# Kernel optimization log

Hardware: AMD Instinct MI355X
Metric: run time of the kernel (lower is better)

The kernel has to match this reference:

```python
import jax, jax.numpy as jnp
import numpy as np

# ContextualAttention config (matches init_kwargs)
KS, STRIDE, DIL, FUSE_K, SCALE = 3, 1, 1, 3, 10.0
B, C, H, W = 2, 128, 64, 64
L = H * W  # number of background patches (SAME padding, stride 1)


def _same_pad(x, k, s):
    # TF-style SAME padding, identical to the repo's same_padding helper
    _, _, h, w = x.shape
    oh, ow = -(-h // s), -(-w // s)
    ph = max(0, (oh - 1) * s + k - h)
    pw = max(0, (ow - 1) * s + k - w)
    return jnp.pad(x, ((0, 0), (0, 0), (ph // 2, ph - ph // 2), (pw // 2, pw - pw // 2)))


def _patches(x, k, s):
    # extract_image_patches: SAME pad + unfold -> [N, L, C*k*k], (c, kh, kw) ordering
    xp = _same_pad(x, k, s)
    n, c, hp, wp = xp.shape
    oh, ow = (hp - k) // s + 1, (wp - k) // s + 1
    cols = jnp.stack(
        [xp[:, :, i:i + (oh - 1) * s + 1:s, j:j + (ow - 1) * s + 1:s]
         for i in range(k) for j in range(k)], axis=2)  # [N, C, k*k, oh, ow]
    return cols.reshape(n, c * k * k, oh * ow).transpose(0, 2, 1)


def _fuse(scores):
    # diagonal fuse-smoothing: conv the [L_b, L_f] score matrix with eye(k), twice
    # (second pass on the transposed spatial layout), exactly as in the torch code
    bn = scores.shape[0]
    eye = jnp.eye(FUSE_K, dtype=scores.dtype)[None, None]  # [1,1,k,k]
    conv = lambda v: jax.lax.conv_general_dilated(
        v, eye, (1, 1), [(1, 1), (1, 1)],
        dimension_numbers=('NCHW', 'OIHW', 'NCHW'))
    y = conv(scores.reshape(bn, 1, L, L))
    y = y.reshape(bn, H, W, H, W).transpose(0, 2, 1, 4, 3).reshape(bn, 1, L, L)
    y = conv(y)
    y = y.reshape(bn, W, H, W, H).transpose(0, 2, 1, 4, 3)  # back to [b,H,W,H,W]
    return y.reshape(bn, L, H, W)


def setup_inputs() -> dict:
    key = jax.random.key(0)
    kf, kb, km = jax.random.split(key, 3)
    f = jax.random.normal(kf, (B, C, H, W), jnp.float32)
    b = jax.random.normal(kb, (B, C, H, W), jnp.float32)
    mask = (jax.random.uniform(km, (1, 1, H, W)) < 0.05).astype(jnp.float32)
    return {"f": f, "b": b, "mask": mask}


def reference(f, b, mask):
    kernel = 2 * DIL  # raw patch size for aggregation (=2)
    # raw background patches used by the transposed-conv aggregation
    raw_w = _patches(b, kernel, DIL * STRIDE).reshape(B, L, C, kernel, kernel)
    # DIL == 1 => F.interpolate(scale=1.0, nearest) is identity on f/b/mask
    w = _patches(b, KS, STRIDE)      # [B, L, C*9] matching patches
    fp = _patches(f, KS, 1)          # [B, Lf, C*9] foreground patches (SAME pad)
    m = _patches(mask, KS, STRIDE)[0]                    # [L, 9]
    mm = (jnp.mean(m, axis=1) == 0.0).astype(f.dtype)    # [L] 1 = patch usable

    # per-patch L2 normalization (clamped at 1e-4), conv-as-similarity == patch GEMM
    wn = w / jnp.maximum(jnp.sqrt(jnp.sum(w * w, axis=2, keepdims=True)), 1e-4)
    scores = jnp.einsum('bkd,bqd->bkq', wn, fp).reshape(B, L, H, W)
    scores = _fuse(scores)

    mmb = mm[None, :, None, None]
    attn = jax.nn.softmax(scores * mmb * SCALE, axis=1) * mmb  # softmax over L

    # conv_transpose2d(attn, raw_w, stride=1, padding=1) == VALID corr with flipped,
    # IO-swapped 2x2 kernel (k-1-p = 0 padding); per-sample weights -> vmap
    def agg(a, rw):  # a: [L,H,W], rw: [L,C,2,2]
        rhs = jnp.flip(rw, axis=(2, 3)).transpose(1, 0, 2, 3)  # [C, L, 2, 2] OIHW
        return jax.lax.conv_general_dilated(
            a[None], rhs, (1, 1), [(0, 0), (0, 0)],
            dimension_numbers=('NCHW', 'OIHW', 'NCHW'))[0]

    y = jax.vmap(agg)(attn, raw_w) / 4.0       # [B, C, H-1, W-1]
    y = jnp.pad(y, ((0, 0), (0, 0), (0, 1), (0, 1)))  # output_padding = DIL % 2 = 1
    return y
```

## Files before the change

kernel.cpp:

```cpp
#include <hip/hip_runtime.h>

#define L 4096
#define HH 64
#define CC 128
#define BB 2

typedef _Float16 f16;
typedef _Float16 f16x8 __attribute__((ext_vector_type(8)));
typedef float f32x4 __attribute__((ext_vector_type(4)));

__device__ __forceinline__ void gl_lds16(const f16* g, f16* l) {
  __builtin_amdgcn_global_load_lds(
      (const __attribute__((address_space(1))) void*)g,
      (__attribute__((address_space(3))) void*)l, 16, 0, 0);
}

__device__ __forceinline__ int sigma_(int j) { return ((j & 63) << 6) | (j >> 6); }

__device__ float fuse9(const f16* __restrict__ Sb, int k, int j) {
  float acc = 0.f;
  int cK = sigma_(k), cQ = sigma_(j);
#pragma unroll
  for (int u = -1; u <= 1; ++u) {
    int a = cK + u, bq = cQ + u;
    if ((unsigned)a < L && (unsigned)bq < L) {
      int r = sigma_(a), c = sigma_(bq);
#pragma unroll
      for (int t = -1; t <= 1; ++t) {
        int rr = r + t, cc = c + t;
        if ((unsigned)rr < L && (unsigned)cc < L) acc += (float)Sb[(size_t)rr * L + cc];
      }
    }
  }
  return acc;
}

__global__ __launch_bounds__(256) void k_repack(
    const float* __restrict__ b, const float* __restrict__ f,
    f16* __restrict__ bT, f16* __restrict__ fT, f16* __restrict__ zp) {
  __shared__ float tile[128][65];
  int u0 = blockIdx.x * 64;
  int z = blockIdx.y;
  int batch = z >> 1;
  const float* src = ((z & 1) ? f : b) + (size_t)batch * CC * L;
  f16* dst = ((z & 1) ? fT : bT) + (size_t)batch * L * CC;
  int tid = threadIdx.x;
  if (blockIdx.x == 0 && z == 0 && tid < 32) zp[tid] = (f16)0.f;
#pragma unroll
  for (int i = 0; i < 32; ++i) {
    int idx = i * 256 + tid;
    int c = idx >> 6, ux = idx & 63;
    tile[c][ux] = src[(size_t)c * L + u0 + ux];
  }
  __syncthreads();
#pragma unroll
  for (int j = 0; j < 4; ++j) {
    int t2 = j * 256 + tid;
    int u = t2 >> 4, ch = t2 & 15;
    f16x8 v;
#pragma unroll
    for (int e = 0; e < 8; ++e) v[e] = (f16)tile[ch * 8 + e][u];
    *(f16x8*)(dst + (size_t)(u0 + u) * CC + ch * 8) = v;
  }
}

__global__ __launch_bounds__(256) void k_ssq(const float* __restrict__ b, float* __restrict__ ssq) {
  int u = blockIdx.x * 256 + threadIdx.x;
  int batch = blockIdx.y;
  const float* bp = b + (size_t)batch * CC * L + u;
  float s = 0.f;
#pragma unroll 4
  for (int c = 0; c < CC; ++c) { float v = bp[(size_t)c * L]; s += v * v; }
  ssq[batch * L + u] = s;
}

__global__ void k_norm(const float* __restrict__ ssq, float* __restrict__ inv_n) {
  int gi = blockIdx.x * 256 + threadIdx.x;
  if (gi >= BB * L) return;
  int batch = gi >> 12, k = gi & (L - 1);
  int ky = k >> 6, kx = k & 63;
  float s = 0.f;
#pragma unroll
  for (int dy = -1; dy <= 1; ++dy)
#pragma unroll
    for (int dx = -1; dx <= 1; ++dx) {
      if ((unsigned)(ky + dy) < 64 && (unsigned)(kx + dx) < 64)
        s += ssq[batch * L + k + dy * 64 + dx];
    }
  inv_n[gi] = 1.f / fmaxf(sqrtf(s), 1e-4f);
}

__global__ __launch_bounds__(256) void k_prep_bm(const float* __restrict__ b, f16* __restrict__ bm) {
  int idx = blockIdx.x * 256 + threadIdx.x;
  int e8 = idx * 8;
  int k0 = e8 & (L - 1);
  int c = (e8 >> 12) & (CC - 1);
  int bt = e8 >> 19;
  int batch = bt & 1;
  int tap = bt >> 1;
  int di = 1 - (tap >> 1), dj = 1 - (tap & 1);
  int ky = k0 >> 6, kx0 = k0 & 63;
  const float* src = b + ((size_t)batch * CC + c) * L + k0 + di * 64 + dj;
  bool rowok = (ky + di) < 64;
  f16x8 v;
#pragma unroll
  for (int e = 0; e < 8; ++e) {
    float x = (rowok && (kx0 + e + dj) < 64) ? src[e] : 0.f;
    v[e] = (f16)x;
  }
  *(f16x8*)(bm + (size_t)e8) = v;
}

__global__ void k_prep_mm(const float* __restrict__ mask, float* __restrict__ mmv) {
  int k = blockIdx.x * 256 + threadIdx.x;
  if (k >= L) return;
  int ky = k >> 6, kx = k & 63;
  float s = 0.f;
  for (int i = 0; i < 3; ++i)
    for (int j = 0; j < 3; ++j) {
      int yy = ky + i - 1, xx = kx + j - 1;
      if (yy >= 0 && yy < 64 && xx >= 0 && xx < 64) s += mask[yy * 64 + xx];
    }
  mmv[k] = (s == 0.f) ? 1.f : 0.f;
}

__global__ void k_zcnt(const float* __restrict__ mmv, float* __restrict__ zcnt) {
  int i = blockIdx.x * 256 + threadIdx.x;
  if (i >= 512) return;
  float s = 0.f;
#pragma unroll
  for (int r = 0; r < 8; ++r) s += (mmv[i * 8 + r] == 0.f) ? 1.f : 0.f;
  zcnt[i] = s;
}

__global__ __launch_bounds__(256) void k_gemm_scores(
    const f16* __restrict__ bT, const f16* __restrict__ fT,
    const float* __restrict__ inv_n, const f16* __restrict__ zp,
    f16* __restrict__ S) {
  __shared__ f16 As[2][128 * 64];
  __shared__ f16 Bs[2][128 * 64];
  int qt = blockIdx.x, kt = blockIdx.y, batch = blockIdx.z;
  int tid = threadIdx.x, wid = tid >> 6, lane = tid & 63;
  int wr = wid >> 1, wc = wid & 1;
  const f16* A0 = bT + (size_t)batch * L * CC;
  const f16* B0 = fT + (size_t)batch * L * CC;
  f32x4 acc[4][4] = {};
  int rA = wr * 64 + (lane & 15);
  int rB = wc * 64 + (lane & 15);

  const f16* baseA_[4]; const f16* baseB_[4];
  int offL_[4];
  unsigned mA_[4], mB_[4];
#pragma unroll
  for (int i = 0; i < 4; ++i) {
    int chunk = (i * 4 + wid) * 64 + lane;
    int row = chunk >> 3;
    int lg = (lane & 7) ^ (row & 7);
    int k = kt * 128 + row;
    int q = qt * 128 + row;
    baseA_[i] = A0 + (size_t)k * CC + lg * 8;
    baseB_[i] = B0 + (size_t)q * CC + lg * 8;
    offL_[i] = chunk * 8;
    int ky = k >> 6, kx = k & 63, qy = q >> 6, qx = q & 63;
    unsigned ma = 0, mb = 0;
#pragma unroll
    for (int rr = 0; rr < 9; ++rr) {
      int dy = rr / 3 - 1, dx = rr - (rr / 3) * 3 - 1;
      if ((unsigned)(ky + dy) < 64u && (unsigned)(kx + dx) < 64u) ma |= 1u << rr;
      if ((unsigned)(qy + dy) < 64u && (unsigned)(qx + dx) < 64u) mb |= 1u << rr;
    }
    mA_[i] = ma; mB_[i] = mb;
  }

#define STAGE_T(tt, bsel)                                                     \
  do {                                                                        \
    int rr_ = (tt) >> 1, half_ = (tt) & 1;                                    \
    int dy_ = rr_ / 3 - 1, dx_ = rr_ - (rr_ / 3) * 3 - 1;                     \
    int doff_ = (dy_ * 64 + dx_) * CC + half_ * 64;                           \
    _Pragma("unroll")                                                         \
    for (int i = 0; i < 4; ++i) {                                             \
      gl_lds16(((mA_[i] >> rr_) & 1u) ? (baseA_[i] + doff_) : zp,             \
               &As[bsel][0] + offL_[i]);                                      \
      gl_lds16(((mB_[i] >> rr_) & 1u) ? (baseB_[i] + doff_) : zp,             \
               &Bs[bsel][0] + offL_[i]);                                      \
    }                                                                         \
  } while (0)

  STAGE_T(0, 0);
  int cur = 0;
#pragma unroll 1
  for (int t = 0; t < 18; ++t) {
    __syncthreads();
    if (t < 17) STAGE_T(t + 1, cur ^ 1);
    const f16* Ab = &As[cur][0];
    const f16* Bb = &Bs[cur][0];
#pragma unroll
    for (int h2 = 0; h2 < 2; ++h2) {
      int cb = h2 * 4 + (lane >> 4);
      f16x8 af[4], bf[4];
#pragma unroll
      for (int m = 0; m < 4; ++m) {
        int row = rA + m * 16;
        af[m] = *(const f16x8*)(Ab + row * 64 + ((cb ^ (row & 7)) * 8));
      }
#pragma unroll
      for (int n = 0; n < 4; ++n) {
        int row = rB + n * 16;
        bf[n] = *(const f16x8*)(Bb + row * 64 + ((cb ^ (row & 7)) * 8));
      }
#pragma unroll
      for (int m = 0; m < 4; ++m)
#pragma unroll
        for (int n = 0; n < 4; ++n)
          acc[m][n] = __builtin_amdgcn_mfma_f32_16x16x32_f16(af[m], bf[n], acc[m][n], 0, 0, 0);
    }
    cur ^= 1;
  }
#undef STAGE_T

  f16* Srow = S + (size_t)batch * L * L;
  int kbase = kt * 128 + wr * 64 + (lane >> 4) * 4;
  int qbase = qt * 128 + wc * 64 + (lane & 15);
#pragma unroll
  for (int m = 0; m < 4; ++m) {
    f32x4 invv = *(const f32x4*)(inv_n + (size_t)batch * L + kbase + m * 16);
#pragma unroll
    for (int r = 0; r < 4; ++r) {
      f16* dst = Srow + (size_t)(kbase + m * 16 + r) * L + qbase;
#pragma unroll
      for (int n = 0; n < 4; ++n) dst[n * 16] = (f16)(acc[m][n][r] * invv[r]);
    }
  }
}

__global__ __launch_bounds__(256) void k_fuse_stats(
    const f16* __restrict__ S, const float* __restrict__ mmv,
    f16* __restrict__ P, float* __restrict__ pmP, float* __restrict__ pl) {
  int tid = threadIdx.x;
  if (tid >= 247) return;
  int jc = blockIdx.x, kc = blockIdx.y, batch = blockIdx.z;
  int g = jc * 247 + tid;
  int q0 = 72 + g * 8;
  const f16* Sb = S + (size_t)batch * L * L;
  f16* Pb = P + (size_t)batch * L * L;
  float lg[8][8];
  float m8[8];
#pragma unroll
  for (int e = 0; e < 8; ++e) m8[e] = -3.0e38f;
  unsigned vmask = 0;
  int k0 = kc * 8;
#pragma unroll
  for (int kk = 0; kk < 8; ++kk) {
    int k = k0 + kk;
    if (mmv[k] == 0.f) continue;
    vmask |= 1u << kk;
    float acc[8] = {0.f, 0.f, 0.f, 0.f, 0.f, 0.f, 0.f, 0.f};
    int cK = sigma_(k);
#pragma unroll
    for (int u = -1; u <= 1; ++u) {
      int a = cK + u;
      if ((unsigned)a >= L) continue;
      int r = sigma_(a);
      const f16* cb = Sb + (size_t)r * L + (q0 + 64 * u);
      {
        f16x8 v = *(const f16x8*)cb;
#pragma unroll
        for (int e = 0; e < 8; ++e) acc[e] += (float)v[e];
      }
      if (r >= 1) {
        const f16* rm = cb - L;
        f16x8 v = *(const f16x8*)rm;
        acc[0] += (float)rm[-1];
#pragma unroll
        for (int e = 1; e < 8; ++e) acc[e] += (float)v[e - 1];
      }
      if (r <= L - 2) {
        const f16* rp = cb + L;
        f16x8 v = *(const f16x8*)rp;
#pragma unroll
        for (int e = 0; e < 7; ++e) acc[e] += (float)v[e + 1];
        acc[7] += (float)rp[8];
      }
    }
#pragma unroll
    for (int e = 0; e < 8; ++e) {
      float x = acc[e] * 10.f;
      lg[kk][e] = x;
      m8[e] = fmaxf(m8[e], x);
    }
  }
  float l8[8] = {0.f, 0.f, 0.f, 0.f, 0.f, 0.f, 0.f, 0.f};
#pragma unroll
  for (int kk = 0; kk < 8; ++kk) {
    if (!((vmask >> kk) & 1u)) continue;
    f16 v[8];
#pragma unroll
    for (int e = 0; e < 8; ++e) {
      float p = __expf(lg[kk][e] - m8[e]);
      l8[e] += p;
      v[e] = (f16)p;
    }
    *(f16x8*)(Pb + (size_t)(k0 + kk) * L + q0) = *(f16x8*)v;
  }
  float* pmp = pmP + (size_t)kc * (BB * L) + (size_t)batch * L + q0;
  float* plp = pl + (size_t)kc * (BB * L) + (size_t)batch * L + q0;
  *(f32x4*)pmp = *(f32x4*)&m8[0]; *(f32x4*)(pmp + 4) = *(f32x4*)&m8[4];
  *(f32x4*)plp = *(f32x4*)&l8[0]; *(f32x4*)(plp + 4) = *(f32x4*)&l8[4];
}

__global__ __launch_bounds__(256) void k_fuse_stats_edge(
    const f16* __restrict__ S, const float* __restrict__ mmv,
    f16* __restrict__ P, float* __restrict__ pmP, float* __restrict__ pl) {
  int tid = threadIdx.x;
  if (tid >= 144) return;
  int q = (tid < 72) ? tid : (4024 + tid - 72);
  int kc = blockIdx.x, batch = blockIdx.y;
  const f16* Sb = S + (size_t)batch * L * L;
  f16* Pb = P + (size_t)batch * L * L;
  float lgs[8];
  float m = -3.0e38f;
  unsigned vmask = 0;
  int k0 = kc * 8;
#pragma unroll
  for (int kk = 0; kk < 8; ++kk) {
    int k = k0 + kk;
    if (mmv[k] == 0.f) continue;
    vmask |= 1u << kk;
    float x = 10.f * fuse9(Sb, k, q);
    lgs[kk] = x;
    m = fmaxf(m, x);
  }
  float l = 0.f;
#pragma unroll
  for (int kk = 0; kk < 8; ++kk) {
    if (!((vmask >> kk) & 1u)) continue;
    float p = __expf(lgs[kk] - m);
    l += p;
    Pb[(size_t)(k0 + kk) * L + q] = (f16)p;
  }
  pmP[(size_t)kc * (BB * L) + (size_t)batch * L + q] = m;
  pl[(size_t)kc * (BB * L) + (size_t)batch * L + q] = l;
}

__global__ __launch_bounds__(256) void k_softmax_reduce(
    const float* __restrict__ pmP, const float* __restrict__ pl,
    const float* __restrict__ zcnt,
    float* __restrict__ Mq, float* __restrict__ invLq) {
  __shared__ float sm[4][64], sl[4][64];
  int tid = threadIdx.x;
  int ql = tid & 63, part = tid >> 6;
  int qi = blockIdx.x * 64 + ql;
  float m = -3.0e38f, l = 0.f;
  int i0 = part * 128;
  float cntp = 0.f;
#pragma unroll 4
  for (int i = i0; i < i0 + 128; ++i) {
    float pmv = pmP[(size_t)i * (BB * L) + qi];
    float plv = pl[(size_t)i * (BB * L) + qi];
    float nm = fmaxf(m, pmv);
    l = l * __expf(m - nm) + plv * __expf(pmv - nm);
    m = nm;
    cntp += zcnt[i & 511];
  }
  if (cntp > 0.f) {
    float nm = fmaxf(m, 0.f);
    l = l * __expf(m - nm) + cntp * __expf(-nm);
    m = nm;
  }
  sm[part][ql] = m; sl[part][ql] = l;
  __syncthreads();
  if (part == 0) {
    float M = sm[0][ql];
#pragma unroll
    for (int p = 1; p < 4; ++p) M = fmaxf(M, sm[p][ql]);
    float Ls = 0.f;
#pragma unroll
    for (int p = 0; p < 4; ++p) Ls += sl[p][ql] * __expf(sm[p][ql] - M);
    Mq[qi] = M;
    invLq[qi] = 1.f / Ls;
  }
}

__global__ __launch_bounds__(512) void k_agg(
    const f16* __restrict__ P, const float* __restrict__ pmP,
    const float* __restrict__ mmv,
    const float* __restrict__ Mq, const float* __restrict__ invLq,
    const f16* __restrict__ bm, float* __restrict__ part) {
  __shared__ f16 Asm[512 * 32];
  __shared__ f16 Bt[136 * 40];
  int pt = blockIdx.x, ks = blockIdx.y, batch = blockIdx.z;
  int p0 = pt * 64;
  int tid = threadIdx.x, wid = tid >> 6, lane = tid & 63;
  int wr = wid >> 1, wc = wid & 1;
  const f16* Pb = P + (size_t)batch * L * L;

  const f16* gA_[4]; f16* lA_[4];
#pragma unroll
  for (int i = 0; i < 4; ++i) {
    int R = wid * 64 + i * 16 + (lane >> 2);
    int tap = R >> 7, c = R & 127;
    int chl = (lane & 3) ^ ((R >> 1) & 3);
    gA_[i] = bm + (((size_t)(tap * 2 + batch) * CC + c) * L) + chl * 8;
    lA_[i] = Asm + R * 32 + (lane & 3) * 8;
  }

  bool act1 = (tid < 32);
  int kg_[2]; bool qok_[2]; float M_[2], iL_[2];
  const f16* tb_[2]; f16* bw_[2];
  size_t bq_[2];
#pragma unroll
  for (int s = 0; s < 2; ++s) {
    int tau = tid + s * 512;
    int ppv = tau % 136, kgv = tau / 136;
    if (tau >= 544) { ppv = 0; kgv = 0; }
    kg_[s] = kgv;
    int q = p0 + ppv;
    bool qok = q < L;
    int qc = qok ? q : (L - 1);
    qok_[s] = qok;
    M_[s] = Mq[(size_t)batch * L + qc];
    iL_[s] = invLq[(size_t)batch * L + qc];
    tb_[s] = Pb + (size_t)(kgv * 8) * L + qc;
    bq_[s] = (size_t)batch * L + qc;
    bw_[s] = Bt + ppv * 40 + ((kgv ^ ((ppv >> 3) & 3)) * 8);
  }

  f16x8 vv_[2];
  int kend = ks * 1024 + 1024;

#define LOADB(K0)                                                             \
  do {                                                                        \
    _Pragma("unroll")                                                         \
    for (int s = 0; s < 2; ++s) {                                             \
      if (s == 1 && !act1) break;                                             \
      const f16* tp = tb_[s] + (size_t)(K0) * L;                              \
      int ck = ((K0) >> 3) + kg_[s];                                          \
      float pmv = pmP[(size_t)ck * (BB * L) + bq_[s]];                        \
      float corr = qok_[s] ? __expf(pmv - M_[s]) * iL_[s] : 0.f;              \
      f32x4 ma = *(const f32x4*)(mmv + (K0) + kg_[s] * 8);                    \
      f32x4 mb = *(const f32x4*)(mmv + (K0) + kg_[s] * 8 + 4);                \
      f16 pv[8];                                                              \
      _Pragma("unroll")                                                       \
      for (int j = 0; j < 8; ++j) pv[j] = tp[(size_t)j * L];                  \
      f16 v[8];                                                               \
      _Pragma("unroll")                                                       \
      for (int j = 0; j < 8; ++j) {                                           \
        float mmj = (j < 4) ? ma[j] : mb[j - 4];                              \
        v[j] = (mmj != 0.f) ? (f16)((float)pv[j] * corr) : (f16)0.f;          \
      }                                                                       \
      vv_[s] = *(f16x8*)v;                                                    \
    }                                                                         \
  } while (0)

  LOADB(ks * 1024);
  f32x4 acc[2][2] = {};
#pragma unroll 1
  for (int k0 = ks * 1024; k0 < kend; k0 += 32) {
    __syncthreads();
    *(f16x8*)bw_[0] = vv_[0];
    if (act1) *(f16x8*)bw_[1] = vv_[1];
#pragma unroll
    for (int i = 0; i < 4; ++i) gl_lds16(gA_[i] + k0, lA_[i]);
    __syncthreads();
#pragma unroll
    for (int tap = 0; tap < 4; ++tap) {
      int dlt = (tap >> 1) * 64 + (tap & 1);
      f16x8 af[2], bf[2];
#pragma unroll
      for (int m = 0; m < 2; ++m) {
        int R = tap * 128 + wr * 32 + m * 16 + (lane & 15);
        int ph = (lane >> 4) ^ ((R >> 1) & 3);
        af[m] = *(const f16x8*)(Asm + R * 32 + ph * 8);
      }
#pragma unroll
      for (int n = 0; n < 2; ++n) {
        int pp = wc * 32 + n * 16 + (lane & 15) + dlt;
        int ph = (lane >> 4) ^ ((pp >> 3) & 3);
        bf[n] = *(const f16x8*)(Bt + pp * 40 + ph * 8);
      }
#pragma unroll
      for (int m = 0; m < 2; ++m)
#pragma unroll
        for (int n = 0; n < 2; ++n)
          acc[m][n] = __builtin_amdgcn_mfma_f32_16x16x32_f16(af[m], bf[n], acc[m][n], 0, 0, 0);
    }
    if (k0 + 32 < kend) LOADB(k0 + 32);
  }
#undef LOADB

  int cb = wr * 32 + (lane >> 4) * 4;
  int pb = p0 + wc * 32 + (lane & 15);
#pragma unroll
  for (int m = 0; m < 2; ++m)
#pragma unroll
    for (int n = 0; n < 2; ++n)
#pragma unroll
      for (int r = 0; r < 4; ++r) {
        int c = cb + m * 16 + r;
        int p = pb + n * 16;
        part[(((size_t)ks * 2 + batch) * CC + c) * L + p] = acc[m][n][r];
      }
}

__global__ __launch_bounds__(256) void k_agg_reduce(const float* __restrict__ part, float* __restrict__ out) {
  int idx = (blockIdx.x * 256 + threadIdx.x) * 4;
  f32x4 s = {0.f, 0.f, 0.f, 0.f};
#pragma unroll
  for (int ks = 0; ks < 4; ++ks) {
    f32x4 v = *(const f32x4*)(part + (size_t)ks * (2 * CC * L) + idx);
#pragma unroll
    for (int e = 0; e < 4; ++e) s[e] += v[e];
  }
  int p = idx & (L - 1);
  int u = p >> 6, vv = p & 63;
  f32x4 o;
#pragma unroll
  for (int e = 0; e < 4; ++e) o[e] = (u < 63 && (vv + e) < 63) ? s[e] * 0.25f : 0.f;
  *(f32x4*)(out + idx) = o;
}

extern "C" void kernel_launch(void* const* d_in, const int* in_sizes, int n_in,
                              void* d_out, int out_size, void* d_ws, size_t ws_size,
                              hipStream_t stream) {
  const float* f = (const float*)d_in[0];
  const float* b = (const float*)d_in[1];
  const float* mask = (const float*)d_in[2];
  float* out = (float*)d_out;
  char* ws = (char*)d_ws;

  f16* P     = (f16*)(ws + 0);
  f16* S     = (f16*)(ws + 67108864);
  f16* bm    = (f16*)(ws + 134217728);
  float* part= (float*)(ws + 142606336);
  float* pmP = (float*)(ws + 159383552);
  float* pl  = (float*)(ws + 176160768);
  float* mmv = (float*)(ws + 192937984);
  float* Mq  = (float*)(ws + 192954368);
  float* iLq = (float*)(ws + 192987136);
  f16* bT    = (f16*)(ws + 193019904);
  f16* fT    = (f16*)(ws + 195117056);
  float* ssq = (float*)(ws + 197214208);
  float* invn= (float*)(ws + 197246976);
  f16* zp    = (f16*)(ws + 197279744);
  float* zcnt= (float*)(ws + 197279872);

  k_repack<<<dim3(64, 4), dim3(256), 0, stream>>>(b, f, bT, fT, zp);
  k_ssq<<<dim3(16, 2), dim3(256), 0, stream>>>(b, ssq);
  k_norm<<<dim3(32), dim3(256), 0, stream>>>(ssq, invn);
  k_prep_bm<<<dim3(2048), dim3(256), 0, stream>>>(b, bm);
  k_prep_mm<<<dim3(16), dim3(256), 0, stream>>>(mask, mmv);
  k_zcnt<<<dim3(2), dim3(256), 0, stream>>>(mmv, zcnt);
  k_gemm_scores<<<dim3(32, 32, 2), dim3(256), 0, stream>>>(bT, fT, invn, zp, S);
  k_fuse_stats<<<dim3(2, 512, 2), dim3(256), 0, stream>>>(S, mmv, P, pmP, pl);
  k_fuse_stats_edge<<<dim3(512, 2), dim3(256), 0, stream>>>(S, mmv, P, pmP, pl);
  k_softmax_reduce<<<dim3(128), dim3(256), 0, stream>>>(pmP, pl, zcnt, Mq, iLq);
  k_agg<<<dim3(64, 4, 2), dim3(512), 0, stream>>>(P, pmP, mmv, Mq, iLq, bm, part);
  k_agg_reduce<<<dim3(1024), dim3(256), 0, stream>>>(part, out);
}
```

Before: 310.4 us.

## Store softmax numerators transposed so aggregation loads contiguous 8-wide vectors

The fuse/stats kernels now write the exponentiated score matrix transposed ([q][k]), with masked entries written as explicit zeros. Each thread loops over 8 key chunks so it can emit 16-byte vector stores along k. The aggregation kernel's B-tile loader becomes a single f16x8 load per thread instead of eight strided scalar loads, and the mask reads are dropped. The cost is that the fuse kernel now writes strided rows (one row per q) and has 8x fewer blocks, each doing more serial work.

```diff
diff --git a/kernel.cpp b/kernel.cpp
--- a/kernel.cpp
+++ b/kernel.cpp
@@ -235,111 +235,133 @@
 
 __global__ __launch_bounds__(256) void k_fuse_stats(
     const f16* __restrict__ S, const float* __restrict__ mmv,
-    f16* __restrict__ P, float* __restrict__ pmP, float* __restrict__ pl) {
+    f16* __restrict__ PT, float* __restrict__ pmP, float* __restrict__ pl) {
   int tid = threadIdx.x;
   if (tid >= 247) return;
-  int jc = blockIdx.x, kc = blockIdx.y, batch = blockIdx.z;
+  int jc = blockIdx.x, kb = blockIdx.y, batch = blockIdx.z;
   int g = jc * 247 + tid;
   int q0 = 72 + g * 8;
   const f16* Sb = S + (size_t)batch * L * L;
-  f16* Pb = P + (size_t)batch * L * L;
-  float lg[8][8];
-  float m8[8];
-#pragma unroll
-  for (int e = 0; e < 8; ++e) m8[e] = -3.0e38f;
-  unsigned vmask = 0;
-  int k0 = kc * 8;
-#pragma unroll
-  for (int kk = 0; kk < 8; ++kk) {
-    int k = k0 + kk;
-    if (mmv[k] == 0.f) continue;
-    vmask |= 1u << kk;
-    float acc[8] = {0.f, 0.f, 0.f, 0.f, 0.f, 0.f, 0.f, 0.f};
-    int cK = sigma_(k);
-#pragma unroll
-    for (int u = -1; u <= 1; ++u) {
-      int a = cK + u;
-      if ((unsigned)a >= L) continue;
-      int r = sigma_(a);
-      const f16* cb = Sb + (size_t)r * L + (q0 + 64 * u);
-      {
-        f16x8 v = *(const f16x8*)cb;
-#pragma unroll
-        for (int e = 0; e < 8; ++e) acc[e] += (float)v[e];
-      }
-      if (r >= 1) {
-        const f16* rm = cb - L;
-        f16x8 v = *(const f16x8*)rm;
-        acc[0] += (float)rm[-1];
-#pragma unroll
-        for (int e = 1; e < 8; ++e) acc[e] += (float)v[e - 1];
-      }
-      if (r <= L - 2) {
-        const f16* rp = cb + L;
-        f16x8 v = *(const f16x8*)rp;
-#pragma unroll
-        for (int e = 0; e < 7; ++e) acc[e] += (float)v[e + 1];
-        acc[7] += (float)rp[8];
+  f16* Pb = PT + (size_t)batch * L * L;
+#pragma unroll 1
+  for (int sc = 0; sc < 8; ++sc) {
+    int k0 = kb * 64 + sc * 8;
+    float lg[8][8];
+    float m8[8];
+#pragma unroll
+    for (int e = 0; e < 8; ++e) m8[e] = -3.0e38f;
+    unsigned vmask = 0;
+#pragma unroll
+    for (int kk = 0; kk < 8; ++kk) {
+      int k = k0 + kk;
+      if (mmv[k] == 0.f) continue;
+      vmask |= 1u << kk;
+      float acc[8] = {0.f, 0.f, 0.f, 0.f, 0.f, 0.f, 0.f, 0.f};
+      int cK = sigma_(k);
+#pragma unroll
+      for (int u = -1; u <= 1; ++u) {
+        int a = cK + u;
+        if ((unsigned)a >= L) continue;
+        int r = sigma_(a);
+        const f16* cb = Sb + (size_t)r * L + (q0 + 64 * u);
+        {
+          f16x8 v = *(const f16x8*)cb;
+#pragma unroll
+          for (int e = 0; e < 8; ++e) acc[e] += (float)v[e];
+        }
+        if (r >= 1) {
+          const f16* rm = cb - L;
+          f16x8 v = *(const f16x8*)rm;
+          acc[0] += (float)rm[-1];
+#pragma unroll
+          for (int e = 1; e < 8; ++e) acc[e] += (float)v[e - 1];
+        }
+        if (r <= L - 2) {
+          const f16* rp = cb + L;
+          f16x8 v = *(const f16x8*)rp;
+#pragma unroll
+          for (int e = 0; e < 7; ++e) acc[e] += (float)v[e + 1];
+          acc[7] += (float)rp[8];
+        }
+      }
+#pragma unroll
+      for (int e = 0; e < 8; ++e) {
+        float x = acc[e] * 10.f;
+        lg[kk][e] = x;
+        m8[e] = fmaxf(m8[e], x);
+      }
+    }
+    float l8[8] = {0.f, 0.f, 0.f, 0.f, 0.f, 0.f, 0.f, 0.f};
+#pragma unroll
+    for (int kk = 0; kk < 8; ++kk) {
+      if ((vmask >> kk) & 1u) {
+#pragma unroll
+        for (int e = 0; e < 8; ++e) {
+          float p = __expf(lg[kk][e] - m8[e]);
+          l8[e] += p;
+          lg[kk][e] = p;
+        }
+      } else {
+#pragma unroll
+        for (int e = 0; e < 8; ++e) lg[kk][e] = 0.f;
       }
     }
 #pragma unroll
     for (int e = 0; e < 8; ++e) {
-      float x = acc[e] * 10.f;
-      lg[kk][e] = x;
-      m8[e] = fmaxf(m8[e], x);
-    }
-  }
-  float l8[8] = {0.f, 0.f, 0.f, 0.f, 0.f, 0.f, 0.f, 0.f};
-#pragma unroll
-  for (int kk = 0; kk < 8; ++kk) {
-    if (!((vmask >> kk) & 1u)) continue;
-    f16 v[8];
-#pragma unroll
-    for (int e = 0; e < 8; ++e) {
-      float p = __expf(lg[kk][e] - m8[e]);
-      l8[e] += p;
-      v[e] = (f16)p;
-    }
-    *(f16x8*)(Pb + (size_t)(k0 + kk) * L + q0) = *(f16x8*)v;
-  }
-  float* pmp = pmP + (size_t)kc * (BB * L) + (size_t)batch * L + q0;
-  float* plp = pl + (size_t)kc * (BB * L) + (size_t)batch * L + q0;
-  *(f32x4*)pmp = *(f32x4*)&m8[0]; *(f32x4*)(pmp + 4) = *(f32x4*)&m8[4];
-  *(f32x4*)plp = *(f32x4*)&l8[0]; *(f32x4*)(plp + 4) = *(f32x4*)&l8[4];
+      f16 v[8];
+#pragma unroll
+      for (int kk = 0; kk < 8; ++kk) v[kk] = (f16)lg[kk][e];
+      *(f16x8*)(Pb + (size_t)(q0 + e) * L + k0) = *(f16x8*)v;
+    }
+    int ck = kb * 8 + sc;
+    float* pmp = pmP + (size_t)ck * (BB * L) + (size_t)batch * L + q0;
+    float* plp = pl + (size_t)ck * (BB * L) + (size_t)batch * L + q0;
+    *(f32x4*)pmp = *(f32x4*)&m8[0]; *(f32x4*)(pmp + 4) = *(f32x4*)&m8[4];
+    *(f32x4*)plp = *(f32x4*)&l8[0]; *(f32x4*)(plp + 4) = *(f32x4*)&l8[4];
+  }
 }
 
 __global__ __launch_bounds__(256) void k_fuse_stats_edge(
     const f16* __restrict__ S, const float* __restrict__ mmv,
-    f16* __restrict__ P, float* __restrict__ pmP, float* __restrict__ pl) {
+    f16* __restrict__ PT, float* __restrict__ pmP, float* __restrict__ pl) {
   int tid = threadIdx.x;
   if (tid >= 144) return;
   int q = (tid < 72) ? tid : (4024 + tid - 72);
-  int kc = blockIdx.x, batch = blockIdx.y;
+  int kb = blockIdx.x, batch = blockIdx.y;
   const f16* Sb = S + (size_t)batch * L * L;
-  f16* Pb = P + (size_t)batch * L * L;
-  float lgs[8];
-  float m = -3.0e38f;
-  unsigned vmask = 0;
-  int k0 = kc * 8;
-#pragma unroll
-  for (int kk = 0; kk < 8; ++kk) {
-    int k = k0 + kk;
-    if (mmv[k] == 0.f) continue;
-    vmask |= 1u << kk;
-    float x = 10.f * fuse9(Sb, k, q);
-    lgs[kk] = x;
-    m = fmaxf(m, x);
-  }
-  float l = 0.f;
-#pragma unroll
-  for (int kk = 0; kk < 8; ++kk) {
-    if (!((vmask >> kk) & 1u)) continue;
-    float p = __expf(lgs[kk] - m);
-    l += p;
-    Pb[(size_t)(k0 + kk) * L + q] = (f16)p;
-  }
-  pmP[(size_t)kc * (BB * L) + (size_t)batch * L + q] = m;
-  pl[(size_t)kc * (BB * L) + (size_t)batch * L + q] = l;
+  f16* Pb = PT + (size_t)batch * L * L;
+#pragma unroll 1
+  for (int sc = 0; sc < 8; ++sc) {
+    int k0 = kb * 64 + sc * 8;
+    float lgs[8];
+    float m = -3.0e38f;
+    unsigned vmask = 0;
+#pragma unroll
+    for (int kk = 0; kk < 8; ++kk) {
+      int k = k0 + kk;
+      if (mmv[k] == 0.f) continue;
+      vmask |= 1u << kk;
+      float x = 10.f * fuse9(Sb, k, q);
+      lgs[kk] = x;
+      m = fmaxf(m, x);
+    }
+    float l = 0.f;
+    f16 v[8];
+#pragma unroll
+    for (int kk = 0; kk < 8; ++kk) {
+      if ((vmask >> kk) & 1u) {
+        float p = __expf(lgs[kk] - m);
+        l += p;
+        v[kk] = (f16)p;
+      } else {
+        v[kk] = (f16)0.f;
+      }
+    }
+    *(f16x8*)(Pb + (size_t)q * L + k0) = *(f16x8*)v;
+    int ck = kb * 8 + sc;
+    pmP[(size_t)ck * (BB * L) + (size_t)batch * L + q] = m;
+    pl[(size_t)ck * (BB * L) + (size_t)batch * L + q] = l;
+  }
 }
 
 __global__ __launch_bounds__(256) void k_softmax_reduce(
@@ -382,8 +404,7 @@
 }
 
 __global__ __launch_bounds__(512) void k_agg(
-    const f16* __restrict__ P, const float* __restrict__ pmP,
-    const float* __restrict__ mmv,
+    const f16* __restrict__ PT, const float* __restrict__ pmP,
     const float* __restrict__ Mq, const float* __restrict__ invLq,
     const f16* __restrict__ bm, float* __restrict__ part) {
   __shared__ f16 Asm[512 * 32];
@@ -392,7 +413,7 @@
   int p0 = pt * 64;
   int tid = threadIdx.x, wid = tid >> 6, lane = tid & 63;
   int wr = wid >> 1, wc = wid & 1;
-  const f16* Pb = P + (size_t)batch * L * L;
+  const f16* Pb = PT + (size_t)batch * L * L;
 
   const f16* gA_[4]; f16* lA_[4];
 #pragma unroll
@@ -406,12 +427,12 @@
 
   bool act1 = (tid < 32);
   int kg_[2]; bool qok_[2]; float M_[2], iL_[2];
-  const f16* tb_[2]; f16* bw_[2];
+  const f16* ptb_[2]; f16* bw_[2];
   size_t bq_[2];
 #pragma unroll
   for (int s = 0; s < 2; ++s) {
     int tau = tid + s * 512;
-    int ppv = tau % 136, kgv = tau / 136;
+    int kgv = tau & 3, ppv = tau >> 2;
     if (tau >= 544) { ppv = 0; kgv = 0; }
     kg_[s] = kgv;
     int q = p0 + ppv;
@@ -420,7 +441,7 @@
     qok_[s] = qok;
     M_[s] = Mq[(size_t)batch * L + qc];
     iL_[s] = invLq[(size_t)batch * L + qc];
-    tb_[s] = Pb + (size_t)(kgv * 8) * L + qc;
+    ptb_[s] = Pb + (size_t)qc * L + kgv * 8;
     bq_[s] = (size_t)batch * L + qc;
     bw_[s] = Bt + ppv * 40 + ((kgv ^ ((ppv >> 3) & 3)) * 8);
   }
@@ -433,21 +454,13 @@
     _Pragma("unroll")                                                         \
     for (int s = 0; s < 2; ++s) {                                             \
       if (s == 1 && !act1) break;                                             \
-      const f16* tp = tb_[s] + (size_t)(K0) * L;                              \
+      f16x8 pv = *(const f16x8*)(ptb_[s] + (K0));                             \
       int ck = ((K0) >> 3) + kg_[s];                                          \
       float pmv = pmP[(size_t)ck * (BB * L) + bq_[s]];                        \
       float corr = qok_[s] ? __expf(pmv - M_[s]) * iL_[s] : 0.f;              \
-      f32x4 ma = *(const f32x4*)(mmv + (K0) + kg_[s] * 8);                    \
-      f32x4 mb = *(const f32x4*)(mmv + (K0) + kg_[s] * 8 + 4);                \
-      f16 pv[8];                                                              \
-      _Pragma("unroll")                                                       \
-      for (int j = 0; j < 8; ++j) pv[j] = tp[(size_t)j * L];                  \
       f16 v[8];                                                               \
       _Pragma("unroll")                                                       \
-      for (int j = 0; j < 8; ++j) {                                           \
-        float mmj = (j < 4) ? ma[j] : mb[j - 4];                              \
-        v[j] = (mmj != 0.f) ? (f16)((float)pv[j] * corr) : (f16)0.f;          \
-      }                                                                       \
+      for (int j = 0; j < 8; ++j) v[j] = (f16)((float)pv[j] * corr);          \
       vv_[s] = *(f16x8*)v;                                                    \
     }                                                                         \
   } while (0)
@@ -528,7 +541,7 @@
   float* out = (float*)d_out;
   char* ws = (char*)d_ws;
 
-  f16* P     = (f16*)(ws + 0);
+  f16* PT    = (f16*)(ws + 0);
   f16* S     = (f16*)(ws + 67108864);
   f16* bm    = (f16*)(ws + 134217728);
   float* part= (float*)(ws + 142606336);
@@ -551,9 +564,9 @@
   k_prep_mm<<<dim3(16), dim3(256), 0, stream>>>(mask, mmv);
   k_zcnt<<<dim3(2), dim3(256), 0, stream>>>(mmv, zcnt);
   k_gemm_scores<<<dim3(32, 32, 2), dim3(256), 0, stream>>>(bT, fT, invn, zp, S);
-  k_fuse_stats<<<dim3(2, 512, 2), dim3(256), 0, stream>>>(S, mmv, P, pmP, pl);
-  k_fuse_stats_edge<<<dim3(512, 2), dim3(256), 0, stream>>>(S, mmv, P, pmP, pl);
+  k_fuse_stats<<<dim3(2, 64, 2), dim3(256), 0, stream>>>(S, mmv, PT, pmP, pl);
+  k_fuse_stats_edge<<<dim3(64, 2), dim3(256), 0, stream>>>(S, mmv, PT, pmP, pl);
   k_softmax_reduce<<<dim3(128), dim3(256), 0, stream>>>(pmP, pl, zcnt, Mq, iLq);
-  k_agg<<<dim3(64, 4, 2), dim3(512), 0, stream>>>(P, pmP, mmv, Mq, iLq, bm, part);
+  k_agg<<<dim3(64, 4, 2), dim3(512), 0, stream>>>(PT, pmP, Mq, iLq, bm, part);
   k_agg_reduce<<<dim3(1024), dim3(256), 0, stream>>>(part, out);
 }
```

Measured after the change: 466.5 us. +50.3%, slower.
